# Kernel tuning notes

Hardware: AMD Instinct MI355X
Metric: run time of the kernel (lower is better)

Reference implementation:

```python
import jax, jax.numpy as jnp
import numpy as np

D_MODEL = 1024
B, S = 4, 4096


def setup_inputs() -> dict:
    key = jax.random.key(0)
    k1, k2, k3, k4, k5 = jax.random.split(key, 5)
    lim = 1.0 / np.sqrt(D_MODEL)  # nn.Linear default init range
    x = jax.random.normal(k1, (B, S, D_MODEL), dtype=jnp.float32)
    mask = jnp.ones((B, S), dtype=jnp.float32)
    W_up = jax.random.uniform(k2, (D_MODEL, D_MODEL), jnp.float32, -lim, lim)
    b_up = jax.random.uniform(k3, (D_MODEL,), jnp.float32, -lim, lim)
    W_f = jax.random.uniform(k4, (D_MODEL, D_MODEL), jnp.float32, -lim, lim)
    b_f = jax.random.uniform(k5, (D_MODEL,), jnp.float32, -lim, lim)
    decay_param = jnp.zeros((1,), dtype=jnp.float32)
    return {"x": x, "mask": mask, "W_up": W_up, "b_up": b_up,
            "W_f": W_f, "b_f": b_f, "decay_param": decay_param}


def _decay_scan(u, decay):
    # h_t = decay * h_{t-1} + u_t  along axis=1, via associative scan.
    # Element: (a, b) representing h -> a*h + b; compose: (a1*a2, b1*a2 + b2).
    a = jnp.broadcast_to(decay, u.shape)

    def combine(c1, c2):
        a1, b1 = c1
        a2, b2 = c2
        return a1 * a2, b1 * a2 + b2

    _, h = jax.lax.associative_scan(combine, (a, u), axis=1)
    return h


def reference(x, mask, W_up, b_up, W_f, b_f, decay_param):
    decay = jax.nn.sigmoid(decay_param)[0]
    # u_i = mask_i * linear_update(x_i)
    u = (jnp.einsum('bsd,ed->bse', x, W_up) + b_up) * mask[..., None]
    # h_t = sum_{i<=t} decay^(t-i) * u_i  (exponential-decay recurrence)
    h = _decay_scan(u, decay)
    return jnp.einsum('bsd,ed->bse', h, W_f) + b_f
```

## Files before the change

kernel.cpp:

```cpp
#include <hip/hip_runtime.h>
#include <hip/hip_bf16.h>
#include <cstdint>
#include <cstddef>

#define DMODEL 1024
#define BATCH  4
#define SEQ    4096
#define BSROWS (BATCH*SEQ)
#define CHUNK  32
#define NCHUNK (SEQ/CHUNK)
#define NCH_T  (BATCH*NCHUNK)

typedef __attribute__((ext_vector_type(8))) short bf16x8;
typedef __attribute__((ext_vector_type(4))) float f32x4;


__device__ __forceinline__ unsigned short f2bf(float f) {
  union { float f; uint32_t u; } v; v.f = f;
  uint32_t u = v.u;
  u += 0x7FFFu + ((u >> 16) & 1u);
  return (unsigned short)(u >> 16);
}

__device__ __forceinline__ float sigmoid_dev(const float* dp) {
  return 1.0f / (1.0f + expf(-dp[0]));
}

typedef __attribute__((address_space(1))) void void_g;
typedef __attribute__((address_space(3))) void void_l;

__device__ __forceinline__ void gl2lds16(const void* g, void* l) {
  __builtin_amdgcn_global_load_lds((void_g*)g, (void_l*)l, 16, 0, 0);
}

__device__ __forceinline__ void kloop64(
    const unsigned short* __restrict__ A, const unsigned short* __restrict__ B,
    int m0, int n0, f32x4 acc[2][2],
    unsigned short* As, unsigned short* Bs, int tid) {
  int lane = tid & 63, w = tid >> 6, wm = w & 1, wn = w >> 1;
  int quad = lane >> 4, l16 = lane & 15;
  int r = tid >> 3, cch = tid & 7;
  int g = cch ^ (r & 7);

  auto stage = [&](int t, int slot) {
    int k0 = t * 64;
    unsigned short* dA = As + slot * 4096;
    unsigned short* dB = Bs + slot * 4096;
    gl2lds16(A + (size_t)(m0 + r) * DMODEL + k0 + g * 8,      dA + r * 64 + cch * 8);
    gl2lds16(A + (size_t)(m0 + 32 + r) * DMODEL + k0 + g * 8, dA + (32 + r) * 64 + cch * 8);
    gl2lds16(B + (size_t)(n0 + r) * DMODEL + k0 + g * 8,      dB + r * 64 + cch * 8);
    gl2lds16(B + (size_t)(n0 + 32 + r) * DMODEL + k0 + g * 8, dB + (32 + r) * 64 + cch * 8);
  };
  auto compute = [&](int slot) {
    const bf16x8* Av = (const bf16x8*)(As + slot * 4096);
    const bf16x8* Bv = (const bf16x8*)(Bs + slot * 4096);
    #pragma unroll
    for (int kk = 0; kk < 2; ++kk) {
      bf16x8 af[2], bfr[2];
      #pragma unroll
      for (int i = 0; i < 2; ++i) {
        int rowA = wm * 32 + i * 16 + l16;
        af[i]  = Av[rowA * 8 + ((kk * 4 + quad) ^ (l16 & 7))];
        int rowB = wn * 32 + i * 16 + l16;
        bfr[i] = Bv[rowB * 8 + ((kk * 4 + quad) ^ (l16 & 7))];
      }
      __builtin_amdgcn_s_setprio(1);
      #pragma unroll
      for (int i = 0; i < 2; ++i)
        #pragma unroll
        for (int j = 0; j < 2; ++j)
          acc[i][j] = __builtin_amdgcn_mfma_f32_16x16x32_bf16(af[i], bfr[j], acc[i][j], 0, 0, 0);
      __builtin_amdgcn_s_setprio(0);
    }
  };

  stage(0, 0); stage(1, 1);
  asm volatile("s_waitcnt vmcnt(4)" ::: "memory");
  __builtin_amdgcn_s_barrier();
  asm volatile("" ::: "memory");
  int cur = 0;
  for (int t = 0; t < 14; ++t) {
    int ns = cur + 2; if (ns >= 3) ns -= 3;
    stage(t + 2, ns);
    compute(cur);
    asm volatile("s_waitcnt vmcnt(4)" ::: "memory");
    __builtin_amdgcn_s_barrier();
    asm volatile("" ::: "memory");
    cur = (cur == 2) ? 0 : cur + 1;
  }
  compute(cur);
  asm volatile("s_waitcnt vmcnt(0)" ::: "memory");
  __builtin_amdgcn_s_barrier();
  asm volatile("" ::: "memory");
  cur = (cur == 2) ? 0 : cur + 1;
  compute(cur);
}

__global__ __launch_bounds__(256) void prep_kernel(
    const float* __restrict__ x, const float* __restrict__ mask,
    const float* __restrict__ W_up, const float* __restrict__ b_up,
    const float* __restrict__ W_f, const float* __restrict__ dp,
    unsigned short* __restrict__ Wf_bf, unsigned short* __restrict__ WupT,
    float* __restrict__ bb, unsigned short* __restrict__ hv,
    float* __restrict__ carry, float* __restrict__ lbeta,
    float* __restrict__ cbeta) {
  __shared__ float tile[32][33];
  int blk = blockIdx.x;
  int tid = threadIdx.x;

  if (blk < 512) {
    float decay = sigmoid_dev(dp);
    int b = blk / NCHUNK, c = blk % NCHUNK;
    int base = b * SEQ + c * CHUNK;
    const float4* xp = (const float4*)(x + (size_t)base * DMODEL);
    const float4* mp4 = (const float4*)(mask + base);
    float mreg[32];
    #pragma unroll
    for (int q = 0; q < 8; ++q) {
      float4 t = mp4[q];
      mreg[q * 4 + 0] = t.x; mreg[q * 4 + 1] = t.y;
      mreg[q * 4 + 2] = t.z; mreg[q * 4 + 3] = t.w;
    }
    float4 h = make_float4(0.f, 0.f, 0.f, 0.f);
    #pragma unroll
    for (int s = 0; s < CHUNK; ++s) {
      float m = mreg[s];
      float4 xv = xp[(size_t)s * (DMODEL / 4) + tid];
      h.x = decay * h.x + m * xv.x;
      h.y = decay * h.y + m * xv.y;
      h.z = decay * h.z + m * xv.z;
      h.w = decay * h.w + m * xv.w;
      ushort4 o;
      o.x = f2bf(h.x); o.y = f2bf(h.y); o.z = f2bf(h.z); o.w = f2bf(h.w);
      ((ushort4*)hv)[(size_t)(base + s) * (DMODEL / 4) + tid] = o;
    }
    ((float4*)carry)[(size_t)blk * (DMODEL / 4) + tid] = h;
  } else if (blk < 1536) {
    int e = blk - 512;
    int lane = tid & 63, w = tid >> 6;
    float4 v = ((const float4*)(W_f + (size_t)e * DMODEL))[tid];
    float4 bu = ((const float4*)b_up)[tid];
    ushort4 o;
    o.x = f2bf(v.x); o.y = f2bf(v.y); o.z = f2bf(v.z); o.w = f2bf(v.w);
    ((ushort4*)(Wf_bf + (size_t)e * DMODEL))[tid] = o;
    float s = v.x * bu.x + v.y * bu.y + v.z * bu.z + v.w * bu.w;
    #pragma unroll
    for (int off = 32; off; off >>= 1) s += __shfl_down(s, off);
    if (lane == 0) ((float*)tile)[w] = s;
    __syncthreads();
    if (tid == 0)
      bb[e] = ((float*)tile)[0] + ((float*)tile)[1] +
              ((float*)tile)[2] + ((float*)tile)[3];
  } else if (blk < 2560) {
    int id = blk - 1536;
    int bx = id & 31, by = id >> 5;
    int tx = tid & 31, ty = tid >> 5;
    int xx = bx * 32 + tx;
    int y0 = by * 32;
    for (int j = ty; j < 32; j += 8)
      tile[j][tx] = W_up[(size_t)(y0 + j) * DMODEL + xx];
    __syncthreads();
    int ox = by * 32 + tx;
    int oy0 = bx * 32;
    for (int j = ty; j < 32; j += 8)
      WupT[(size_t)(oy0 + j) * DMODEL + ox] = f2bf(tile[tx][j]);
  } else {
    float decay = sigmoid_dev(dp);
    int t = (blk - 2560) * 256 + tid;
    int s = t & 31;
    int cbase = t & ~31;
    float hb = 0.f;
    for (int i = 0; i <= s; ++i)
      hb = decay * hb + mask[cbase + i];
    lbeta[t] = hb;
    if (s == 31) cbeta[t >> 5] = hb;
  }
}

__global__ __launch_bounds__(256) void mid2_kernel(
    const unsigned short* __restrict__ Wf_bf,
    const unsigned short* __restrict__ WupT,
    unsigned short* __restrict__ Wc,
    const float* __restrict__ carry, const float* __restrict__ cbeta,
    const float* __restrict__ dp,
    unsigned short* __restrict__ Pbf, float* __restrict__ pbeta) {
  __shared__ unsigned short As[3 * 64 * 64];
  __shared__ unsigned short Bs[3 * 64 * 64];
  int tid = threadIdx.x;
  if (blockIdx.x < 256) {
    int mt = blockIdx.x >> 4, nt = blockIdx.x & 15;
    f32x4 acc[2][2] = {};
    kloop64(Wf_bf, WupT, mt * 64, nt * 64, acc, As, Bs, tid);
    int lane = tid & 63, w = tid >> 6, wm = w & 1, wn = w >> 1;
    int quad = lane >> 4, l16 = lane & 15;
    #pragma unroll
    for (int j = 0; j < 2; ++j) {
      int col = nt * 64 + wn * 32 + j * 16 + l16;
      #pragma unroll
      for (int i = 0; i < 2; ++i) {
        int rowb = mt * 64 + wm * 32 + i * 16 + quad * 4;
        #pragma unroll
        for (int rr = 0; rr < 4; ++rr)
          Wc[(size_t)(rowb + rr) * DMODEL + col] = f2bf(acc[i][j][rr]);
      }
    }
  } else {
    float decay = sigmoid_dev(dp);
    float dL = powf(decay, (float)CHUNK);
    int gid = (blockIdx.x - 256) * 256 + tid;
    int b = gid >> 10, dd = gid & 1023;
    float P = 0.f;
    for (int c0 = 0; c0 < NCHUNK; c0 += 8) {
      float v[8];
      #pragma unroll
      for (int j = 0; j < 8; ++j)
        v[j] = carry[(size_t)(b * NCHUNK + c0 + j) * DMODEL + dd];
      #pragma unroll
      for (int j = 0; j < 8; ++j) {
        Pbf[(size_t)(b * NCHUNK + c0 + j) * DMODEL + dd] = f2bf(P);
        P = dL * P + v[j];
      }
    }
    if (dd == 0) {
      float Pb = 0.f;
      for (int c0 = 0; c0 < NCHUNK; c0 += 16) {
        float v[16];
        #pragma unroll
        for (int j = 0; j < 16; ++j) v[j] = cbeta[b * NCHUNK + c0 + j];
        #pragma unroll
        for (int j = 0; j < 16; ++j) {
          pbeta[b * NCHUNK + c0 + j] = Pb;
          Pb = dL * Pb + v[j];
        }
      }
    }
  }
}

__global__ __launch_bounds__(256) void pout_kernel(
    const unsigned short* __restrict__ Pbf,
    const unsigned short* __restrict__ Wc,
    const float* __restrict__ pbeta, const float* __restrict__ bb,
    float* __restrict__ Pout) {
  __shared__ unsigned short As[3 * 64 * 64];
  __shared__ unsigned short Bs[3 * 64 * 64];
  int tid = threadIdx.x;
  int mt = blockIdx.x >> 4, nt = blockIdx.x & 15;
  f32x4 acc[2][2] = {};
  kloop64(Pbf, Wc, mt * 64, nt * 64, acc, As, Bs, tid);
  int lane = tid & 63, w = tid >> 6, wm = w & 1, wn = w >> 1;
  int quad = lane >> 4, l16 = lane & 15;
  #pragma unroll
  for (int j = 0; j < 2; ++j) {
    int col = nt * 64 + wn * 32 + j * 16 + l16;
    float bbv = bb[col];
    #pragma unroll
    for (int i = 0; i < 2; ++i) {
      int rowb = mt * 64 + wm * 32 + i * 16 + quad * 4;
      #pragma unroll
      for (int rr = 0; rr < 4; ++rr) {
        int row = rowb + rr;
        Pout[(size_t)row * DMODEL + col] = acc[i][j][rr] + pbeta[row] * bbv;
      }
    }
  }
}

__global__ __launch_bounds__(256) void gemm_main(
    const unsigned short* __restrict__ A,
    const unsigned short* __restrict__ Bm,
    const float* __restrict__ Pout,
    const float* __restrict__ lbeta,
    const float* __restrict__ bb,
    const float* __restrict__ bias_f,
    const float* __restrict__ dp,
    float* __restrict__ out) {
  __shared__ unsigned short As[3 * 128 * 32];
  __shared__ unsigned short Bs[3 * 128 * 32];
  __shared__ float dpow[CHUNK];
  int tid = threadIdx.x;
  if (tid < CHUNK) {
    float decay = sigmoid_dev(dp);
    dpow[tid] = powf(decay, (float)(tid + 1));
  }
  __syncthreads();
  int lane = tid & 63, w = tid >> 6, wm = w & 1, wn = w >> 1;
  int quad = lane >> 4, l16 = lane & 15;
  int r = tid >> 2;
  int c4 = tid & 3;
  int g = c4 ^ ((r >> 1) & 3);
  int phi = (l16 >> 1) & 3;
  int m0 = (blockIdx.x & 127) * 128;
  int n0 = (blockIdx.x >> 7) * 128;
  f32x4 acc[4][4] = {};

  auto stage = [&](int t, int slot) {
    int k0 = t * 32;
    unsigned short* dA = As + slot * (128 * 32);
    unsigned short* dB = Bs + slot * (128 * 32);
    gl2lds16(A  + (size_t)(m0 + r) * DMODEL + k0 + g * 8,       dA + r * 32 + c4 * 8);
    gl2lds16(A  + (size_t)(m0 + 64 + r) * DMODEL + k0 + g * 8,  dA + (64 + r) * 32 + c4 * 8);
    gl2lds16(Bm + (size_t)(n0 + r) * DMODEL + k0 + g * 8,       dB + r * 32 + c4 * 8);
    gl2lds16(Bm + (size_t)(n0 + 64 + r) * DMODEL + k0 + g * 8,  dB + (64 + r) * 32 + c4 * 8);
  };
  auto compute = [&](int slot) {
    const bf16x8* Av = (const bf16x8*)(As + slot * (128 * 32));
    const bf16x8* Bv = (const bf16x8*)(Bs + slot * (128 * 32));
    bf16x8 af[4], bfr[4];
    #pragma unroll
    for (int i = 0; i < 4; ++i) {
      int rowA = wm * 64 + i * 16 + l16;
      af[i]  = Av[rowA * 4 + (quad ^ phi)];
      int rowB = wn * 64 + i * 16 + l16;
      bfr[i] = Bv[rowB * 4 + (quad ^ phi)];
    }
    __builtin_amdgcn_s_setprio(1);
    #pragma unroll
    for (int i = 0; i < 4; ++i)
      #pragma unroll
      for (int j = 0; j < 4; ++j)
        acc[i][j] = __builtin_amdgcn_mfma_f32_16x16x32_bf16(af[i], bfr[j], acc[i][j], 0, 0, 0);
    __builtin_amdgcn_s_setprio(0);
  };

  stage(0, 0); stage(1, 1);
  asm volatile("s_waitcnt vmcnt(4)" ::: "memory");
  __builtin_amdgcn_s_barrier();
  asm volatile("" ::: "memory");
  int cur = 0;
  for (int t = 0; t < 30; ++t) {
    int ns = cur + 2; if (ns >= 3) ns -= 3;
    stage(t + 2, ns);
    compute(cur);
    asm volatile("s_waitcnt vmcnt(4)" ::: "memory");
    __builtin_amdgcn_s_barrier();
    asm volatile("" ::: "memory");
    cur = (cur == 2) ? 0 : cur + 1;
  }
  compute(cur);
  asm volatile("s_waitcnt vmcnt(0)" ::: "memory");
  __builtin_amdgcn_s_barrier();
  asm volatile("" ::: "memory");
  cur = (cur == 2) ? 0 : cur + 1;
  compute(cur);

  float bbv[4], bfv[4];
  #pragma unroll
  for (int j = 0; j < 4; ++j) {
    int col = n0 + wn * 64 + j * 16 + l16;
    bbv[j] = bb[col];
    bfv[j] = bias_f[col];
  }
  #pragma unroll
  for (int i = 0; i < 4; ++i) {
    #pragma unroll
    for (int rr = 0; rr < 4; ++rr) {
      int row = m0 + wm * 64 + i * 16 + quad * 4 + rr;
      float lb  = lbeta[row];
      float dpw = dpow[row & 31];
      const float* poRow = Pout + (size_t)(row >> 5) * DMODEL;
      float* outRow = out + (size_t)row * DMODEL;
      #pragma unroll
      for (int j = 0; j < 4; ++j) {
        int col = n0 + wn * 64 + j * 16 + l16;
        outRow[col] = acc[i][j][rr] + dpw * poRow[col] + lb * bbv[j] + bfv[j];
      }
    }
  }
}


extern "C" void kernel_launch(void* const* d_in, const int* in_sizes, int n_in,
                              void* d_out, int out_size, void* d_ws, size_t ws_size,
                              hipStream_t stream) {
  const float* x    = (const float*)d_in[0];
  const float* mask = (const float*)d_in[1];
  const float* W_up = (const float*)d_in[2];
  const float* b_up = (const float*)d_in[3];
  const float* W_f  = (const float*)d_in[4];
  const float* b_f  = (const float*)d_in[5];
  const float* dp   = (const float*)d_in[6];
  float* out = (float*)d_out;

  char* ws = (char*)d_ws;
  unsigned short* hv    = (unsigned short*)(ws);
  unsigned short* Wc    = (unsigned short*)(ws + 33554432);
  unsigned short* Wf_bf = (unsigned short*)(ws + 35651584);
  unsigned short* WupT  = (unsigned short*)(ws + 37748736);
  float* carry  = (float*)(ws + 39845888);
  unsigned short* Pbf = (unsigned short*)(ws + 41943040);
  float* Pout   = (float*)(ws + 42991616);
  float* lbeta  = (float*)(ws + 45088768);
  float* cbeta  = (float*)(ws + 45154304);
  float* pbeta  = (float*)(ws + 45156352);
  float* bb     = (float*)(ws + 45158400);

  prep_kernel<<<2624, 256, 0, stream>>>(x, mask, W_up, b_up, W_f, dp,
                                        Wf_bf, WupT, bb, hv, carry, lbeta, cbeta);
  mid2_kernel<<<272, 256, 0, stream>>>(Wf_bf, WupT, Wc, carry, cbeta, dp,
                                       Pbf, pbeta);
  pout_kernel<<<128, 256, 0, stream>>>(Pbf, Wc, pbeta, bb, Pout);
  gemm_main<<<1024, 256, 0, stream>>>(hv, Wc, Pout, lbeta, bb, b_f, dp, out);
}
```

Baseline: 201.2 us.

## Enlarge main GEMM tile to 256x256 with 8 waves and 4-stage pipeline

The main GEMM moves from 128x128 tiles with 4 waves and a 3-slot LDS ring to 256x256 tiles with 8 waves (each wave holding a 128x64 sub-tile) and a 4-slot ring. Loads of A and B are split and interleaved with two MFMA phases per k-step, and a block-to-XCD mapping keeps m-tiles local to each XCD. The goal is higher arithmetic intensity and L2 reuse. In exchange it uses more LDS and registers per block, and the grid shrinks to 256 blocks, which may underfill the 256 CUs or reduce occupancy.

```diff
diff --git a/kernel.cpp b/kernel.cpp
--- a/kernel.cpp
+++ b/kernel.cpp
@@ -266,7 +266,7 @@
   }
 }
 
-__global__ __launch_bounds__(256) void gemm_main(
+__global__ __launch_bounds__(512) void gemm_main(
     const unsigned short* __restrict__ A,
     const unsigned short* __restrict__ Bm,
     const float* __restrict__ Pout,
@@ -275,74 +275,98 @@
     const float* __restrict__ bias_f,
     const float* __restrict__ dp,
     float* __restrict__ out) {
-  __shared__ unsigned short As[3 * 128 * 32];
-  __shared__ unsigned short Bs[3 * 128 * 32];
+  __shared__ unsigned short As[4 * 256 * 32];
+  __shared__ unsigned short Bs[4 * 256 * 32];
   __shared__ float dpow[CHUNK];
+  const int SLOT = 256 * 32;
   int tid = threadIdx.x;
   if (tid < CHUNK) {
     float decay = sigmoid_dev(dp);
     dpow[tid] = powf(decay, (float)(tid + 1));
   }
   __syncthreads();
-  int lane = tid & 63, w = tid >> 6, wm = w & 1, wn = w >> 1;
+
+  int lane = tid & 63, wid = tid >> 6;
+  int wm = wid >> 2, wn = wid & 3;
   int quad = lane >> 4, l16 = lane & 15;
-  int r = tid >> 2;
-  int c4 = tid & 3;
+  int phi = (l16 >> 1) & 3;
+  int r = tid >> 2, c4 = tid & 3;
   int g = c4 ^ ((r >> 1) & 3);
-  int phi = (l16 >> 1) & 3;
-  int m0 = (blockIdx.x & 127) * 128;
-  int n0 = (blockIdx.x >> 7) * 128;
-  f32x4 acc[4][4] = {};
-
-  auto stage = [&](int t, int slot) {
+
+  int bid = blockIdx.x;
+  int xcd = bid & 7, jb = bid >> 3;
+  int m0 = (xcd * 8 + (jb >> 2)) * 256;
+  int n0 = (jb & 3) * 256;
+
+  f32x4 acc[8][4] = {};
+
+  auto stageA = [&](int t, int slot) {
     int k0 = t * 32;
-    unsigned short* dA = As + slot * (128 * 32);
-    unsigned short* dB = Bs + slot * (128 * 32);
-    gl2lds16(A  + (size_t)(m0 + r) * DMODEL + k0 + g * 8,       dA + r * 32 + c4 * 8);
-    gl2lds16(A  + (size_t)(m0 + 64 + r) * DMODEL + k0 + g * 8,  dA + (64 + r) * 32 + c4 * 8);
+    unsigned short* dA = As + slot * SLOT;
+    gl2lds16(A + (size_t)(m0 + r) * DMODEL + k0 + g * 8,        dA + r * 32 + c4 * 8);
+    gl2lds16(A + (size_t)(m0 + 128 + r) * DMODEL + k0 + g * 8,  dA + (128 + r) * 32 + c4 * 8);
+  };
+  auto stageB = [&](int t, int slot) {
+    int k0 = t * 32;
+    unsigned short* dB = Bs + slot * SLOT;
     gl2lds16(Bm + (size_t)(n0 + r) * DMODEL + k0 + g * 8,       dB + r * 32 + c4 * 8);
-    gl2lds16(Bm + (size_t)(n0 + 64 + r) * DMODEL + k0 + g * 8,  dB + (64 + r) * 32 + c4 * 8);
+    gl2lds16(Bm + (size_t)(n0 + 128 + r) * DMODEL + k0 + g * 8, dB + (128 + r) * 32 + c4 * 8);
   };
-  auto compute = [&](int slot) {
-    const bf16x8* Av = (const bf16x8*)(As + slot * (128 * 32));
-    const bf16x8* Bv = (const bf16x8*)(Bs + slot * (128 * 32));
-    bf16x8 af[4], bfr[4];
+
+  bf16x8 bfr[4];
+  auto phase = [&](int slot, int mh, bool loadB) {
+    const bf16x8* Av = (const bf16x8*)(As + slot * SLOT);
+    const bf16x8* Bv = (const bf16x8*)(Bs + slot * SLOT);
+    bf16x8 af[4];
     #pragma unroll
     for (int i = 0; i < 4; ++i) {
-      int rowA = wm * 64 + i * 16 + l16;
-      af[i]  = Av[rowA * 4 + (quad ^ phi)];
-      int rowB = wn * 64 + i * 16 + l16;
-      bfr[i] = Bv[rowB * 4 + (quad ^ phi)];
+      int rowA = wm * 128 + mh * 64 + i * 16 + l16;
+      af[i] = Av[rowA * 4 + (quad ^ phi)];
+    }
+    if (loadB) {
+      #pragma unroll
+      for (int j = 0; j < 4; ++j) {
+        int rowB = wn * 64 + j * 16 + l16;
+        bfr[j] = Bv[rowB * 4 + (quad ^ phi)];
+      }
     }
     __builtin_amdgcn_s_setprio(1);
     #pragma unroll
     for (int i = 0; i < 4; ++i)
       #pragma unroll
       for (int j = 0; j < 4; ++j)
-        acc[i][j] = __builtin_amdgcn_mfma_f32_16x16x32_bf16(af[i], bfr[j], acc[i][j], 0, 0, 0);
+        acc[mh * 4 + i][j] =
+            __builtin_amdgcn_mfma_f32_16x16x32_bf16(af[i], bfr[j], acc[mh * 4 + i][j], 0, 0, 0);
     __builtin_amdgcn_s_setprio(0);
   };
 
-  stage(0, 0); stage(1, 1);
+  stageA(0, 0); stageB(0, 0);
+  stageA(1, 1); stageB(1, 1);
+  stageA(2, 2); stageB(2, 2);
+  asm volatile("s_waitcnt vmcnt(8)" ::: "memory");
+  __builtin_amdgcn_s_barrier();
+  asm volatile("" ::: "memory");
+
+  for (int t = 0; t < 29; ++t) {
+    int cs = t & 3;
+    int ss = (t + 3) & 3;
+    stageA(t + 3, ss);
+    phase(cs, 0, true);
+    stageB(t + 3, ss);
+    phase(cs, 1, false);
+    asm volatile("s_waitcnt vmcnt(8)" ::: "memory");
+    __builtin_amdgcn_s_barrier();
+    asm volatile("" ::: "memory");
+  }
+  phase(1, 0, true);  phase(1, 1, false);
   asm volatile("s_waitcnt vmcnt(4)" ::: "memory");
   __builtin_amdgcn_s_barrier();
   asm volatile("" ::: "memory");
-  int cur = 0;
-  for (int t = 0; t < 30; ++t) {
-    int ns = cur + 2; if (ns >= 3) ns -= 3;
-    stage(t + 2, ns);
-    compute(cur);
-    asm volatile("s_waitcnt vmcnt(4)" ::: "memory");
-    __builtin_amdgcn_s_barrier();
-    asm volatile("" ::: "memory");
-    cur = (cur == 2) ? 0 : cur + 1;
-  }
-  compute(cur);
+  phase(2, 0, true);  phase(2, 1, false);
   asm volatile("s_waitcnt vmcnt(0)" ::: "memory");
   __builtin_amdgcn_s_barrier();
   asm volatile("" ::: "memory");
-  cur = (cur == 2) ? 0 : cur + 1;
-  compute(cur);
+  phase(3, 0, true);  phase(3, 1, false);
 
   float bbv[4], bfv[4];
   #pragma unroll
@@ -352,10 +376,10 @@
     bfv[j] = bias_f[col];
   }
   #pragma unroll
-  for (int i = 0; i < 4; ++i) {
+  for (int i = 0; i < 8; ++i) {
     #pragma unroll
     for (int rr = 0; rr < 4; ++rr) {
-      int row = m0 + wm * 64 + i * 16 + quad * 4 + rr;
+      int row = m0 + wm * 128 + i * 16 + quad * 4 + rr;
       float lb  = lbeta[row];
       float dpw = dpow[row & 31];
       const float* poRow = Pout + (size_t)(row >> 5) * DMODEL;
@@ -400,5 +424,5 @@
   mid2_kernel<<<272, 256, 0, stream>>>(Wf_bf, WupT, Wc, carry, cbeta, dp,
                                        Pbf, pbeta);
   pout_kernel<<<128, 256, 0, stream>>>(Pbf, Wc, pbeta, bb, Pout);
-  gemm_main<<<1024, 256, 0, stream>>>(hv, Wc, Pout, lbeta, bb, b_f, dp, out);
-}
+  gemm_main<<<256, 512, 0, stream>>>(hv, Wc, Pout, lbeta, bb, b_f, dp, out);
+}
```

Measured after the change: 189.6 us. 1.06x faster.
